# Kernel optimization log

Measured on AMD Instinct MI355X. Metric: run time of the kernel, lower is better.

The kernel has to match this reference:

```python
import jax, jax.numpy as jnp
import numpy as np

N_NODES = 50000
N_EDGES = 800000
EMB = 384            # EMBEDDING_DIM
NODE_F = EMB + 4     # 388
EDGE_F = EMB + 1     # 385
HEADS = 2
HID = 32             # per-head out_channels
HC = HEADS * HID     # 64
EDGE_IN = 2 * HC + EMB  # 512 classifier input
NEG_SLOPE = 0.2


def setup_inputs() -> dict:
    key = jax.random.key(0)
    ks = jax.random.split(key, 16)
    s = 0.05
    return {
        "x": jax.random.normal(ks[0], (N_NODES, NODE_F), dtype=jnp.float32),
        "edge_index": jax.random.randint(ks[1], (2, N_EDGES), 0, N_NODES, dtype=jnp.int32),
        "edge_attr": jax.random.uniform(ks[2], (N_EDGES, EDGE_F), dtype=jnp.float32),
        # GATv2Conv params
        "lin_l_w": jax.random.normal(ks[3], (NODE_F, HC), dtype=jnp.float32) * s,
        "lin_l_b": jnp.zeros((HC,), jnp.float32),
        "lin_r_w": jax.random.normal(ks[4], (NODE_F, HC), dtype=jnp.float32) * s,
        "lin_r_b": jnp.zeros((HC,), jnp.float32),
        "lin_e_w": jax.random.normal(ks[5], (EDGE_F, HC), dtype=jnp.float32) * s,
        "att": jax.random.normal(ks[6], (HEADS, HID), dtype=jnp.float32) * s,
        "conv_b": jnp.zeros((HC,), jnp.float32),
        # edge classifier MLP
        "mlp1_w": jax.random.normal(ks[7], (EDGE_IN, 64), dtype=jnp.float32) * s,
        "mlp1_b": jnp.zeros((64,), jnp.float32),
        "mlp2_w": jax.random.normal(ks[8], (64, 3), dtype=jnp.float32) * s,
        "mlp2_b": jnp.zeros((3,), jnp.float32),
    }


def _gatv2(x, edge_index, edge_attr, lin_l_w, lin_l_b, lin_r_w, lin_r_b,
           lin_e_w, att, conv_b):
    N = x.shape[0]
    src, tgt = edge_index[0], edge_index[1]
    # PyG add_self_loops with fill_value='mean': self-loop edge_attr is the
    # mean of incoming edge attributes per target node (0 if none).
    ones = jnp.ones((edge_attr.shape[0],), edge_attr.dtype)
    cnt = jax.ops.segment_sum(ones, tgt, num_segments=N)
    loop_attr = jax.ops.segment_sum(edge_attr, tgt, num_segments=N)
    loop_attr = loop_attr / jnp.maximum(cnt, 1.0)[:, None]
    ar = jnp.arange(N, dtype=src.dtype)
    src = jnp.concatenate([src, ar])
    tgt = jnp.concatenate([tgt, ar])
    ea = jnp.concatenate([edge_attr, loop_attr], axis=0)  # [E+N, EDGE_F]

    xl = (x @ lin_l_w + lin_l_b).reshape(N, HEADS, HID)  # source transform
    xr = (x @ lin_r_w + lin_r_b).reshape(N, HEADS, HID)  # target transform
    ee = (ea @ lin_e_w).reshape(-1, HEADS, HID)

    # GATv2 scoring: att . leaky_relu(x_j + x_i + e_ij)
    m = jax.nn.leaky_relu(xl[src] + xr[tgt] + ee, NEG_SLOPE)  # [E', H, C]
    score = jnp.einsum('ehc,hc->eh', m, att)                  # [E', H]
    # segment softmax over incoming edges of each target node
    smax = jax.ops.segment_max(score, tgt, num_segments=N)
    ex = jnp.exp(score - smax[tgt])
    ssum = jax.ops.segment_sum(ex, tgt, num_segments=N)
    alpha = ex / (ssum[tgt] + 1e-16)                          # [E', H]
    out = jax.ops.segment_sum(alpha[:, :, None] * xl[src], tgt, num_segments=N)
    return out.reshape(N, HC) + conv_b


def reference(x, edge_index, edge_attr, lin_l_w, lin_l_b, lin_r_w, lin_r_b,
              lin_e_w, att, conv_b, mlp1_w, mlp1_b, mlp2_w, mlp2_b):
    h = jax.nn.relu(_gatv2(x, edge_index, edge_attr, lin_l_w, lin_l_b,
                           lin_r_w, lin_r_b, lin_e_w, att, conv_b))
    # prediction edges == graph edges; query emb = edge_attr[:, :-1]
    src_e = h[edge_index[0]]
    tgt_e = h[edge_index[1]]
    q = edge_attr[:, :-1]
    e = jnp.concatenate([src_e, tgt_e, q], axis=1)  # [E, 512]
    e = jax.nn.relu(e @ mlp1_w + mlp1_b)
    logits = e @ mlp2_w + mlp2_b                    # [E, 3]
    probs = jax.nn.softmax(logits, axis=1)
    trust = 0.0 * probs[:, 0] + 0.5 * probs[:, 1] + 1.0 * probs[:, 2]
    return trust
```

## Files before the change

kernel.cpp:

```cpp
#include <hip/hip_runtime.h>

#define N_NODES 50000
#define N_EDGES 800000
#define NODE_F  388
#define EDGE_F  385
#define HC      64
#define KRED    384
#define NKT     6
#define NB      196

#define O_XLB     0L
#define O_XRB     1600000L
#define O_HAB     3200000L
#define O_HBB     4800000L
#define O_EESUM   6400000L
#define O_SSUM    9600000L
#define O_WSUM    9700000L
#define O_DEG     12900000L
#define O_CURSOR  12950000L
#define O_ROWPTR  13010000L
#define O_BSUM    13070000L
#define O_CSRE    13080000L
#define O_CSRS    13880000L
#define O_CSRT    14680000L
#define O_WT      15500000L
#define O_WT2     15530000L
#define O_QW      15560000L

typedef __attribute__((ext_vector_type(8))) short bf8;
typedef __attribute__((ext_vector_type(4))) float f4;

typedef __attribute__((address_space(1))) const unsigned char ga_u8;
typedef __attribute__((address_space(3))) unsigned char lds_u8;

static __device__ __forceinline__ void gload_lds16(const void* g, void* l) {
    __builtin_amdgcn_global_load_lds((ga_u8*)g, (lds_u8*)l, 16, 0, 0);
}

static __device__ __forceinline__ unsigned short f2bf(float f) {
    unsigned u = __float_as_uint(f);
    u += 0x7FFFu + ((u >> 16) & 1u);
    return (unsigned short)(u >> 16);
}
static __device__ __forceinline__ float bf2f(unsigned short h) {
    return __uint_as_float(((unsigned)h) << 16);
}
static __device__ __forceinline__ unsigned cvtpk(float lo, float hi) {
    unsigned r;
    asm("v_cvt_pk_bf16_f32 %0, %1, %2" : "=v"(r) : "v"(lo), "v"(hi));
    return r;
}
static __device__ __forceinline__ void raw_barrier() {
    __builtin_amdgcn_sched_barrier(0);
    __builtin_amdgcn_s_barrier();
    __builtin_amdgcn_sched_barrier(0);
}

__global__ __launch_bounds__(256) void k_prep(
    const float* __restrict__ we, const float* __restrict__ w1,
    const float* __restrict__ wl, const float* __restrict__ wr,
    unsigned short* __restrict__ wt, unsigned short* __restrict__ wt2)
{
    int half = blockIdx.x / 96;
    int gid = (blockIdx.x - half * 96) * 256 + threadIdx.x;
    int c  = gid / 192;
    int k  = 2 * (gid - c * 192);
    float f0, f1;
    if (half == 0) {
        if (c < HC) {
            f0 = we[(long)k * HC + c];
            f1 = we[(long)(k + 1) * HC + c];
        } else {
            f0 = w1[(long)(128 + k) * HC + (c - HC)];
            f1 = w1[(long)(128 + k + 1) * HC + (c - HC)];
        }
        *(unsigned*)(wt + (long)c * KRED + k) =
            (unsigned)f2bf(f0) | ((unsigned)f2bf(f1) << 16);
    } else {
        const float* w = (c < HC) ? wl : wr;
        int cc = (c < HC) ? c : c - HC;
        f0 = w[(long)k * HC + cc];
        f1 = w[(long)(k + 1) * HC + cc];
        *(unsigned*)(wt2 + (long)c * KRED + k) =
            (unsigned)f2bf(f0) | ((unsigned)f2bf(f1) << 16);
    }
}

__global__ __launch_bounds__(256, 5) void k_node_lin(
    const float* __restrict__ x, const unsigned short* __restrict__ wt2,
    const float* __restrict__ wl, const float* __restrict__ wr,
    const float* __restrict__ bl, const float* __restrict__ br,
    unsigned short* __restrict__ xlb, unsigned short* __restrict__ xrb)
{
    __shared__ __align__(16) char W_s[2][16384];
    const int t = threadIdx.x;
    const int l = t & 63;
    const int w = t >> 6;
    const int n0 = blockIdx.x * 64;
    const int rb = (w & 1) * 32;
    const int cb = (w >> 1) * 64;
    const int lr = l & 15;
    const int lk = l >> 4;

    int wsrc[4];
#pragma unroll
    for (int i = 0; i < 4; ++i) {
        int c = w * 32 + i * 8 + (l >> 3);
        wsrc[i] = c * (KRED * 2) + ((((l & 7) * 16)) ^ ((l >> 3) << 4));
    }
    const char* wtb = (const char*)wt2;

    long rowx[2];
#pragma unroll
    for (int rg = 0; rg < 2; ++rg) {
        int n = n0 + rb + rg * 16 + lr;
        if (n >= N_NODES) n = N_NODES - 1;
        rowx[rg] = (long)n * NODE_F;
    }

    float af[2][16];
    bf8 fa[2][2];
    f4 acc[2][4];
#pragma unroll
    for (int rg = 0; rg < 2; ++rg)
#pragma unroll
        for (int cg = 0; cg < 4; ++cg) acc[rg][cg] = (f4)(0.f);

#define STAGE_W(kt, buf)                                                         \
    {                                                                            \
        _Pragma("unroll")                                                        \
        for (int i = 0; i < 4; ++i)                                              \
            gload_lds16(wtb + wsrc[i] + (kt) * 128, &W_s[buf][w * 4096 + i * 1024]); \
    }
#define ISSUE_AX(kt)                                                             \
    {                                                                            \
        _Pragma("unroll")                                                        \
        for (int rg = 0; rg < 2; ++rg) {                                         \
            const float* rp = x + rowx[rg] + (kt) * 64 + lk * 8;                 \
            float4 a0 = *(const float4*)(rp);                                    \
            float4 a1 = *(const float4*)(rp + 4);                                \
            float4 a2 = *(const float4*)(rp + 32);                               \
            float4 a3 = *(const float4*)(rp + 36);                               \
            af[rg][0]=a0.x; af[rg][1]=a0.y; af[rg][2]=a0.z; af[rg][3]=a0.w;      \
            af[rg][4]=a1.x; af[rg][5]=a1.y; af[rg][6]=a1.z; af[rg][7]=a1.w;      \
            af[rg][8]=a2.x; af[rg][9]=a2.y; af[rg][10]=a2.z; af[rg][11]=a2.w;    \
            af[rg][12]=a3.x; af[rg][13]=a3.y; af[rg][14]=a3.z; af[rg][15]=a3.w;  \
        }                                                                        \
    }
#define CVT_AX()                                                                 \
    {                                                                            \
        _Pragma("unroll")                                                        \
        for (int rg = 0; rg < 2; ++rg)                                           \
            _Pragma("unroll")                                                    \
            for (int ks = 0; ks < 2; ++ks) {                                     \
                union { bf8 v; unsigned u[4]; } tu;                              \
                _Pragma("unroll")                                                \
                for (int p = 0; p < 4; ++p)                                      \
                    tu.u[p] = cvtpk(af[rg][ks * 8 + 2 * p], af[rg][ks * 8 + 2 * p + 1]); \
                fa[rg][ks] = tu.v;                                               \
            }                                                                    \
    }

    STAGE_W(0, 0);
    ISSUE_AX(0);

    for (int kt = 0; kt < NKT; ++kt) {
        const int buf = kt & 1;
        CVT_AX();
        if (kt < NKT - 1) { STAGE_W(kt + 1, buf ^ 1); ISSUE_AX(kt + 1); }
        raw_barrier();
        __builtin_amdgcn_s_setprio(1);
#pragma unroll
        for (int ks = 0; ks < 2; ++ks) {
            const int kb = ks * 64 + lk * 16;
#pragma unroll
            for (int cg = 0; cg < 4; ++cg) {
                const int c = cb + cg * 16 + lr;
                bf8 b = *(bf8*)(&W_s[buf][c * 128 + (kb ^ ((c & 7) << 4))]);
                acc[0][cg] = __builtin_amdgcn_mfma_f32_16x16x32_bf16(fa[0][ks], b, acc[0][cg], 0, 0, 0);
                acc[1][cg] = __builtin_amdgcn_mfma_f32_16x16x32_bf16(fa[1][ks], b, acc[1][cg], 0, 0, 0);
            }
        }
        __builtin_amdgcn_s_setprio(0);
        raw_barrier();
    }

    const float* wsf = (cb == 0) ? wl : wr;
    const float* bsf = (cb == 0) ? bl : br;
    unsigned short* dst = (cb == 0) ? xlb : xrb;
    float wtail[4][4], bias[4];
#pragma unroll
    for (int cg = 0; cg < 4; ++cg) {
        int c = cg * 16 + lr;
        bias[cg] = bsf[c];
#pragma unroll
        for (int j = 0; j < 4; ++j)
            wtail[j][cg] = wsf[(long)(KRED + j) * HC + c];
    }
#pragma unroll
    for (int rg = 0; rg < 2; ++rg)
#pragma unroll
    for (int r = 0; r < 4; ++r) {
        const int n = n0 + rb + rg * 16 + lk * 4 + r;
        const int nc = (n < N_NODES) ? n : N_NODES - 1;
        float4 xt = *(const float4*)(x + (long)nc * NODE_F + KRED);
#pragma unroll
        for (int cg = 0; cg < 4; ++cg) {
            float v = acc[rg][cg][r] + bias[cg]
                    + xt.x * wtail[0][cg] + xt.y * wtail[1][cg]
                    + xt.z * wtail[2][cg] + xt.w * wtail[3][cg];
            float nb = __shfl_xor(v, 1);
            if (!(lr & 1) && n < N_NODES)
                *(unsigned*)&dst[(long)n * HC + cg * 16 + lr] = cvtpk(v, nb);
        }
    }
#undef STAGE_W
#undef ISSUE_AX
#undef CVT_AX
}

__global__ __launch_bounds__(256) void k_hist(const int* __restrict__ ei, int* __restrict__ deg)
{
    int e = blockIdx.x * 256 + threadIdx.x;
    if (e < N_EDGES) atomicAdd(&deg[ei[N_EDGES + e]], 1);
}

__global__ __launch_bounds__(256) void k_scan_bsum(const int* __restrict__ deg, int* __restrict__ bsum)
{
    __shared__ int red[4];
    int i = blockIdx.x * 256 + threadIdx.x;
    int v = (i < N_NODES) ? deg[i] : 0;
    for (int m = 1; m < 64; m <<= 1) v += __shfl_xor(v, m);
    if ((threadIdx.x & 63) == 0) red[threadIdx.x >> 6] = v;
    __syncthreads();
    if (threadIdx.x == 0) bsum[blockIdx.x] = red[0] + red[1] + red[2] + red[3];
}

__global__ __launch_bounds__(256) void k_scan_boff(int* bsum)
{
    __shared__ int sc[256];
    int t = threadIdx.x;
    int v = (t < NB) ? bsum[t] : 0;
    sc[t] = v; __syncthreads();
    for (int off = 1; off < 256; off <<= 1) {
        int tv = (t >= off) ? sc[t - off] : 0;
        __syncthreads();
        sc[t] += tv;
        __syncthreads();
    }
    if (t < NB) bsum[t] = sc[t] - v;
}

__global__ __launch_bounds__(256) void k_scan_row(const int* __restrict__ deg,
                                                  const int* __restrict__ bsum,
                                                  int* __restrict__ rowptr)
{
    __shared__ int sc[256];
    int t = threadIdx.x;
    int i = blockIdx.x * 256 + t;
    int v = (i < N_NODES) ? deg[i] : 0;
    sc[t] = v; __syncthreads();
    for (int off = 1; off < 256; off <<= 1) {
        int tv = (t >= off) ? sc[t - off] : 0;
        __syncthreads();
        sc[t] += tv;
        __syncthreads();
    }
    if (i < N_NODES) rowptr[i] = bsum[blockIdx.x] + sc[t] - v;
    if (i == N_NODES - 1) rowptr[N_NODES] = N_EDGES;
}

__global__ __launch_bounds__(256) void k_scatter(const int* __restrict__ ei,
                                                 const int* __restrict__ rowptr,
                                                 int* __restrict__ cursor,
                                                 int* __restrict__ csr_e, int* __restrict__ csr_s,
                                                 int* __restrict__ csr_t)
{
    int e = blockIdx.x * 256 + threadIdx.x;
    if (e >= N_EDGES) return;
    int g = ei[N_EDGES + e];
    int pos = rowptr[g] + atomicAdd(&cursor[g], 1);
    csr_e[pos] = e;
    csr_s[pos] = ei[e];
    csr_t[pos] = g;
}

__global__ __launch_bounds__(256, 4) void k_edge_main(
    const float* __restrict__ ea,
    const int* __restrict__ csr_e, const int* __restrict__ csr_s, const int* __restrict__ csr_t,
    const unsigned short* __restrict__ wt, const float* __restrict__ we,
    const unsigned short* __restrict__ xlb, const unsigned short* __restrict__ xrb,
    const float* __restrict__ att,
    float* __restrict__ eesum, float* __restrict__ ssum, float* __restrict__ wsum,
    unsigned short* __restrict__ qWP)
{
    __shared__ __align__(16) char lds[32768];
    const int t = threadIdx.x;
    const int l = t & 63;
    const int w = t >> 6;
    const long pb = (long)blockIdx.x * 64;
    const int rb = (w & 1) * 32;
    const int cb = (w >> 1) * 64;
    const int lr = l & 15;
    const int lk = l >> 4;

    int wsrc[4];
#pragma unroll
    for (int i = 0; i < 4; ++i) {
        int c = w * 32 + i * 8 + (l >> 3);
        wsrc[i] = c * (KRED * 2) + ((((l & 7) * 16)) ^ ((l >> 3) << 4));
    }
    const char* wtb = (const char*)wt;

    unsigned rowb[2];
#pragma unroll
    for (int rg = 0; rg < 2; ++rg) {
        int e = csr_e[pb + rb + rg * 16 + lr];
        rowb[rg] = (unsigned)e * EDGE_F;
    }

    float af[2][2][16];
    bf8 fa[2][2];
    f4 acc[2][4];
#pragma unroll
    for (int rg = 0; rg < 2; ++rg)
#pragma unroll
        for (int cg = 0; cg < 4; ++cg) acc[rg][cg] = (f4)(0.f);

#define STAGE_W(kt, buf)                                                         \
    {                                                                            \
        _Pragma("unroll")                                                        \
        for (int i = 0; i < 4; ++i)                                              \
            gload_lds16(wtb + wsrc[i] + (kt) * 128,                              \
                        &lds[(buf) * 16384 + w * 4096 + i * 1024]);              \
    }

#define ISSUE_A(b, kt)                                                           \
    {                                                                            \
        _Pragma("unroll")                                                        \
        for (int rg = 0; rg < 2; ++rg) {                                         \
            const float* rp = ea + rowb[rg] + (kt) * 64 + lk * 8;                \
            _Pragma("unroll")                                                    \
            for (int q4 = 0; q4 < 4; ++q4)                                       \
                __builtin_memcpy(&af[b][rg][q4 * 4],                             \
                                 rp + (q4 >> 1) * 32 + (q4 & 1) * 4, 16);        \
        }                                                                        \
    }

#define CVT_A(b)                                                                 \
    {                                                                            \
        _Pragma("unroll")                                                        \
        for (int rg = 0; rg < 2; ++rg)                                           \
            _Pragma("unroll")                                                    \
            for (int ks = 0; ks < 2; ++ks) {                                     \
                union { bf8 v; unsigned u[4]; } tu;                              \
                _Pragma("unroll")                                                \
                for (int p = 0; p < 4; ++p)                                      \
                    tu.u[p] = cvtpk(af[b][rg][ks * 8 + 2 * p],                   \
                                    af[b][rg][ks * 8 + 2 * p + 1]);              \
                fa[rg][ks] = tu.v;                                               \
            }                                                                    \
    }

    STAGE_W(0, 0); ISSUE_A(0, 0);
    STAGE_W(1, 1); ISSUE_A(1, 1);

    for (int kt = 0; kt < NKT; ++kt) {
        const int sl = kt & 1;
        CVT_A(sl);
        raw_barrier();
        __builtin_amdgcn_s_setprio(1);
#pragma unroll
        for (int ks = 0; ks < 2; ++ks) {
            const int kb = ks * 64 + lk * 16;
#pragma unroll
            for (int cg = 0; cg < 4; ++cg) {
                const int c = cb + cg * 16 + lr;
                bf8 b = *(bf8*)(&lds[sl * 16384 + c * 128 + (kb ^ ((c & 7) << 4))]);
                acc[0][cg] = __builtin_amdgcn_mfma_f32_16x16x32_bf16(fa[0][ks], b, acc[0][cg], 0, 0, 0);
                acc[1][cg] = __builtin_amdgcn_mfma_f32_16x16x32_bf16(fa[1][ks], b, acc[1][cg], 0, 0, 0);
            }
        }
        __builtin_amdgcn_s_setprio(0);
        raw_barrier();
        if (kt + 2 < NKT) {
            STAGE_W(kt + 2, sl);
            ISSUE_A(sl, kt + 2);
        }
    }

    float (*ee_s)[65] = (float(*)[65])lds;
    int*   tgt_s      = (int*)(lds + 16640);
    float (*ex_s)[2]  = (float(*)[2])(lds + 16896);

    if (cb == 0) {
        float attv[4], w384[4];
#pragma unroll
        for (int cg = 0; cg < 4; ++cg) {
            attv[cg] = att[cg * 16 + lr];
            w384[cg] = we[(long)(EDGE_F - 1) * HC + cg * 16 + lr];
        }
#pragma unroll
        for (int rg = 0; rg < 2; ++rg)
#pragma unroll
        for (int r = 0; r < 4; ++r) {
            const int row = rb + rg * 16 + lk * 4 + r;
            const long p = pb + row;
            const int s = csr_s[p];
            const int g = csr_t[p];
            const float a384 = ea[(long)csr_e[p] * EDGE_F + (EDGE_F - 1)];
            float sc0 = 0.f, sc1 = 0.f;
#pragma unroll
            for (int cg = 0; cg < 4; ++cg) {
                const int c = cg * 16 + lr;
                float eev = fmaf(a384, w384[cg], acc[rg][cg][r]);
                ee_s[row][c] = eev;
                float m = eev + bf2f(xlb[(long)s * HC + c]) + bf2f(xrb[(long)g * HC + c]);
                float lv = m > 0.f ? m : 0.2f * m;
                float tm = lv * attv[cg];
                if (cg < 2) sc0 += tm; else sc1 += tm;
            }
            sc0 += __shfl_xor(sc0, 1); sc0 += __shfl_xor(sc0, 2);
            sc0 += __shfl_xor(sc0, 4); sc0 += __shfl_xor(sc0, 8);
            sc1 += __shfl_xor(sc1, 1); sc1 += __shfl_xor(sc1, 2);
            sc1 += __shfl_xor(sc1, 4); sc1 += __shfl_xor(sc1, 8);
            if (lr == 0) {
                ex_s[row][0] = __expf(sc0);
                tgt_s[row] = g;
            } else if (lr == 1) {
                ex_s[row][1] = __expf(sc1);
            }
        }
    } else {
#pragma unroll
        for (int rg = 0; rg < 2; ++rg)
#pragma unroll
        for (int r = 0; r < 4; ++r) {
            const long p = pb + rb + rg * 16 + lk * 4 + r;
#pragma unroll
            for (int cg = 0; cg < 4; ++cg) {
                float v = acc[rg][cg][r];
                float nb = __shfl_xor(v, 1);
                if (!(lr & 1)) {
                    unsigned pk = cvtpk(v, nb);
                    *(unsigned*)&qWP[p * HC + cg * 16 + lr] = pk;
                }
            }
        }
    }
    __syncthreads();

    {
        const int c = t & 63;
        const int q = t >> 6;
        const int r0 = q * 16;
        int   cur = tgt_s[r0];
        float run = ee_s[r0][c];
        for (int r = r0 + 1; r < r0 + 16; ++r) {
            int tg = tgt_s[r];
            if (tg != cur) {
                atomicAdd(&eesum[(long)cur * HC + c], run);
                run = 0.f; cur = tg;
            }
            run += ee_s[r][c];
        }
        atomicAdd(&eesum[(long)cur * HC + c], run);
        if (c < 2) {
            int   cur2 = tgt_s[r0];
            float run2 = ex_s[r0][c];
            for (int r = r0 + 1; r < r0 + 16; ++r) {
                int tg = tgt_s[r];
                if (tg != cur2) {
                    atomicAdd(&ssum[(long)cur2 * 2 + c], run2);
                    run2 = 0.f; cur2 = tg;
                }
                run2 += ex_s[r][c];
            }
            atomicAdd(&ssum[(long)cur2 * 2 + c], run2);
        }
    }
    __syncthreads();

    if (cb == 0) {
#pragma unroll
        for (int rg = 0; rg < 2; ++rg)
#pragma unroll
        for (int r = 0; r < 4; ++r) {
            const int row = rb + rg * 16 + lk * 4 + r;
            const long p = pb + row;
            const int s = csr_s[p];
            const float ex0 = ex_s[row][0];
            const float ex1 = ex_s[row][1];
#pragma unroll
            for (int cg = 0; cg < 4; ++cg) {
                const int c = cg * 16 + lr;
                float xv = bf2f(xlb[(long)s * HC + c]);
                ee_s[row][c] = (cg < 2 ? ex0 : ex1) * xv;
            }
        }
    }
    __syncthreads();

    {
        const int c = t & 63;
        const int q = t >> 6;
        const int r0 = q * 16;
        int   cur = tgt_s[r0];
        float run = ee_s[r0][c];
        for (int r = r0 + 1; r < r0 + 16; ++r) {
            int tg = tgt_s[r];
            if (tg != cur) {
                atomicAdd(&wsum[(long)cur * HC + c], run);
                run = 0.f; cur = tg;
            }
            run += ee_s[r][c];
        }
        atomicAdd(&wsum[(long)cur * HC + c], run);
    }
#undef STAGE_W
#undef ISSUE_A
#undef CVT_A
}

__global__ __launch_bounds__(256) void k_node_agg(
    const int* __restrict__ rowptr,
    const float* __restrict__ eesum, const float* __restrict__ ssum,
    const float* __restrict__ wsum,
    const unsigned short* __restrict__ xlb, const unsigned short* __restrict__ xrb,
    const float* __restrict__ att, const float* __restrict__ convb,
    const float* __restrict__ w1,
    unsigned short* __restrict__ hAb, unsigned short* __restrict__ hBb)
{
    const int lane = threadIdx.x & 63;
    const int n = blockIdx.x * 4 + (threadIdx.x >> 6);
    if (n >= N_NODES) return;
    const int h = lane >> 5;
    const int deg = rowptr[n + 1] - rowptr[n];

    float eeS = eesum[(long)n * HC + lane] / (deg > 0 ? (float)deg : 1.f);
    float sex = ssum[(long)n * 2 + h];

    float xlv = bf2f(xlb[(long)n * HC + lane]);
    float v = xlv + bf2f(xrb[(long)n * HC + lane]) + eeS;
    float lv = v > 0.f ? v : 0.2f * v;
    float partial = lv * att[lane];
    partial += __shfl_xor(partial, 1);
    partial += __shfl_xor(partial, 2);
    partial += __shfl_xor(partial, 4);
    partial += __shfl_xor(partial, 8);
    partial += __shfl_xor(partial, 16);
    float exSelf = __expf(partial);
    float inv = 1.f / (sex + exSelf + 1e-16f);
    float aggr = (exSelf * xlv + wsum[(long)n * HC + lane]) * inv;

    float hv = fmaxf(aggr + convb[lane], 0.f);
    float accA = 0.f, accB = 0.f;
    for (int k = 0; k < 64; ++k) {
        float hb = __shfl(hv, k);
        accA = fmaf(hb, w1[k * HC + lane], accA);
        accB = fmaf(hb, w1[(64 + k) * HC + lane], accB);
    }
    hAb[(long)n * HC + lane] = f2bf(accA);
    hBb[(long)n * HC + lane] = f2bf(accB);
}

__global__ __launch_bounds__(256) void k_trust(
    const int* __restrict__ csr_e, const int* __restrict__ csr_s, const int* __restrict__ csr_t,
    const unsigned short* __restrict__ hAb, const unsigned short* __restrict__ hBb,
    const unsigned short* __restrict__ qWP, const float* __restrict__ b1,
    const float* __restrict__ w2, const float* __restrict__ b2,
    float* __restrict__ out)
{
    const long p = (long)blockIdx.x * 256 + threadIdx.x;
    const int s = csr_s[p];
    const int g = csr_t[p];
    const uint4* ha = (const uint4*)(hAb + (long)s * HC);
    const uint4* hb = (const uint4*)(hBb + (long)g * HC);
    const uint4* qw = (const uint4*)(qWP + p * HC);
    float a0 = 0.f, a1 = 0.f, a2 = 0.f;
#pragma unroll
    for (int ch = 0; ch < 8; ++ch) {
        uint4 ua = ha[ch], ub = hb[ch], uq = qw[ch];
        const unsigned* pa = (const unsigned*)&ua;
        const unsigned* pbb = (const unsigned*)&ub;
        const unsigned* pq = (const unsigned*)&uq;
#pragma unroll
        for (int j = 0; j < 4; ++j) {
            const int c = ch * 8 + j * 2;
            unsigned va = pa[j], vb = pbb[j], vq = pq[j];
            float m0 = __uint_as_float(va << 16) + __uint_as_float(vb << 16)
                     + __uint_as_float(vq << 16) + b1[c];
            float m1 = __uint_as_float(va & 0xffff0000u) + __uint_as_float(vb & 0xffff0000u)
                     + __uint_as_float(vq & 0xffff0000u) + b1[c + 1];
            m0 = fmaxf(m0, 0.f);
            m1 = fmaxf(m1, 0.f);
            a0 = fmaf(m0, w2[c * 3 + 0], a0); a0 = fmaf(m1, w2[c * 3 + 3], a0);
            a1 = fmaf(m0, w2[c * 3 + 1], a1); a1 = fmaf(m1, w2[c * 3 + 4], a1);
            a2 = fmaf(m0, w2[c * 3 + 2], a2); a2 = fmaf(m1, w2[c * 3 + 5], a2);
        }
    }
    float l0 = a0 + b2[0], l1 = a1 + b2[1], l2 = a2 + b2[2];
    float mx = fmaxf(l0, fmaxf(l1, l2));
    float e0 = __expf(l0 - mx), e1 = __expf(l1 - mx), e2 = __expf(l2 - mx);
    out[csr_e[p]] = (0.5f * e1 + e2) / (e0 + e1 + e2);
}

extern "C" void kernel_launch(void* const* d_in, const int* in_sizes, int n_in,
                              void* d_out, int out_size, void* d_ws, size_t ws_size,
                              hipStream_t stream)
{
    (void)in_sizes; (void)n_in; (void)out_size; (void)ws_size;
    const float* x     = (const float*)d_in[0];
    const int*   ei    = (const int*)  d_in[1];
    const float* ea    = (const float*)d_in[2];
    const float* wl    = (const float*)d_in[3];
    const float* bl    = (const float*)d_in[4];
    const float* wr    = (const float*)d_in[5];
    const float* br    = (const float*)d_in[6];
    const float* we    = (const float*)d_in[7];
    const float* att   = (const float*)d_in[8];
    const float* convb = (const float*)d_in[9];
    const float* w1    = (const float*)d_in[10];
    const float* b1    = (const float*)d_in[11];
    const float* w2    = (const float*)d_in[12];
    const float* b2    = (const float*)d_in[13];

    float* ws = (float*)d_ws;
    unsigned short* xlb = (unsigned short*)(ws + O_XLB);
    unsigned short* xrb = (unsigned short*)(ws + O_XRB);
    unsigned short* hAb = (unsigned short*)(ws + O_HAB);
    unsigned short* hBb = (unsigned short*)(ws + O_HBB);
    float* eesum  = ws + O_EESUM;
    float* ssum   = ws + O_SSUM;
    float* wsum   = ws + O_WSUM;
    unsigned short* wt  = (unsigned short*)(ws + O_WT);
    unsigned short* wt2 = (unsigned short*)(ws + O_WT2);
    int* deg    = (int*)(ws + O_DEG);
    int* cursor = (int*)(ws + O_CURSOR);
    int* rowptr = (int*)(ws + O_ROWPTR);
    int* bsum   = (int*)(ws + O_BSUM);
    int* csr_e  = (int*)(ws + O_CSRE);
    int* csr_s  = (int*)(ws + O_CSRS);
    int* csr_t  = (int*)(ws + O_CSRT);
    unsigned short* qWP = (unsigned short*)(ws + O_QW);
    float* out  = (float*)d_out;

    hipMemsetAsync(ws + O_EESUM, 0, (size_t)(13000000L - O_EESUM) * sizeof(float), stream);

    k_prep<<<192, 256, 0, stream>>>(we, w1, wl, wr, wt, wt2);
    k_hist<<<3125, 256, 0, stream>>>(ei, deg);
    k_scan_bsum<<<NB, 256, 0, stream>>>(deg, bsum);
    k_scan_boff<<<1, 256, 0, stream>>>(bsum);
    k_scan_row<<<NB, 256, 0, stream>>>(deg, bsum, rowptr);
    k_scatter<<<3125, 256, 0, stream>>>(ei, rowptr, cursor, csr_e, csr_s, csr_t);
    k_node_lin<<<782, 256, 0, stream>>>(x, wt2, wl, wr, bl, br, xlb, xrb);
    k_edge_main<<<N_EDGES / 64, 256, 0, stream>>>(ea, csr_e, csr_s, csr_t, wt, we,
                                                  xlb, xrb, att, eesum, ssum, wsum, qWP);
    k_node_agg<<<N_NODES / 4, 256, 0, stream>>>(rowptr, eesum, ssum, wsum,
                                                xlb, xrb, att, convb, w1, hAb, hBb);
    k_trust<<<3125, 256, 0, stream>>>(csr_e, csr_s, csr_t, hAb, hBb, qWP,
                                      b1, w2, b2, out);
}
```

Before: 749.5 us.

## Merge prep/hist and scan kernels, pack CSR arrays into int4 records

```diff
diff --git a/kernel.cpp b/kernel.cpp
--- a/kernel.cpp
+++ b/kernel.cpp
@@ -20,12 +20,10 @@
 #define O_CURSOR  12950000L
 #define O_ROWPTR  13010000L
 #define O_BSUM    13070000L
-#define O_CSRE    13080000L
-#define O_CSRS    13880000L
-#define O_CSRT    14680000L
-#define O_WT      15500000L
-#define O_WT2     15530000L
-#define O_QW      15560000L
+#define O_CSREST  13080000L
+#define O_WT      16300000L
+#define O_WT2     16330000L
+#define O_QW      16360000L
 
 typedef __attribute__((ext_vector_type(8))) short bf8;
 typedef __attribute__((ext_vector_type(4))) float f4;
@@ -56,11 +54,18 @@
     __builtin_amdgcn_sched_barrier(0);
 }
 
-__global__ __launch_bounds__(256) void k_prep(
+__global__ __launch_bounds__(256) void k_prep_hist(
     const float* __restrict__ we, const float* __restrict__ w1,
     const float* __restrict__ wl, const float* __restrict__ wr,
-    unsigned short* __restrict__ wt, unsigned short* __restrict__ wt2)
-{
+    const int* __restrict__ ei,
+    unsigned short* __restrict__ wt, unsigned short* __restrict__ wt2,
+    int* __restrict__ deg)
+{
+    if (blockIdx.x >= 192) {
+        int e = (blockIdx.x - 192) * 256 + threadIdx.x;
+        if (e < N_EDGES) atomicAdd(&deg[ei[N_EDGES + e]], 1);
+        return;
+    }
     int half = blockIdx.x / 96;
     int gid = (blockIdx.x - half * 96) * 256 + threadIdx.x;
     int c  = gid / 192;
@@ -219,12 +224,6 @@
 #undef CVT_AX
 }
 
-__global__ __launch_bounds__(256) void k_hist(const int* __restrict__ ei, int* __restrict__ deg)
-{
-    int e = blockIdx.x * 256 + threadIdx.x;
-    if (e < N_EDGES) atomicAdd(&deg[ei[N_EDGES + e]], 1);
-}
-
 __global__ __launch_bounds__(256) void k_scan_bsum(const int* __restrict__ deg, int* __restrict__ bsum)
 {
     __shared__ int red[4];
@@ -236,58 +235,45 @@
     if (threadIdx.x == 0) bsum[blockIdx.x] = red[0] + red[1] + red[2] + red[3];
 }
 
-__global__ __launch_bounds__(256) void k_scan_boff(int* bsum)
+__global__ __launch_bounds__(256) void k_scan_row(const int* __restrict__ deg,
+                                                  const int* __restrict__ bsum,
+                                                  int* __restrict__ rowptr)
 {
     __shared__ int sc[256];
+    __shared__ int red[4];
     int t = threadIdx.x;
-    int v = (t < NB) ? bsum[t] : 0;
+    int bv = (t < NB && t < (int)blockIdx.x) ? bsum[t] : 0;
+    for (int m = 1; m < 64; m <<= 1) bv += __shfl_xor(bv, m);
+    if ((t & 63) == 0) red[t >> 6] = bv;
+    int i = blockIdx.x * 256 + t;
+    int v = (i < N_NODES) ? deg[i] : 0;
     sc[t] = v; __syncthreads();
+    int base = red[0] + red[1] + red[2] + red[3];
     for (int off = 1; off < 256; off <<= 1) {
         int tv = (t >= off) ? sc[t - off] : 0;
         __syncthreads();
         sc[t] += tv;
         __syncthreads();
     }
-    if (t < NB) bsum[t] = sc[t] - v;
-}
-
-__global__ __launch_bounds__(256) void k_scan_row(const int* __restrict__ deg,
-                                                  const int* __restrict__ bsum,
-                                                  int* __restrict__ rowptr)
-{
-    __shared__ int sc[256];
-    int t = threadIdx.x;
-    int i = blockIdx.x * 256 + t;
-    int v = (i < N_NODES) ? deg[i] : 0;
-    sc[t] = v; __syncthreads();
-    for (int off = 1; off < 256; off <<= 1) {
-        int tv = (t >= off) ? sc[t - off] : 0;
-        __syncthreads();
-        sc[t] += tv;
-        __syncthreads();
-    }
-    if (i < N_NODES) rowptr[i] = bsum[blockIdx.x] + sc[t] - v;
+    if (i < N_NODES) rowptr[i] = base + sc[t] - v;
     if (i == N_NODES - 1) rowptr[N_NODES] = N_EDGES;
 }
 
 __global__ __launch_bounds__(256) void k_scatter(const int* __restrict__ ei,
                                                  const int* __restrict__ rowptr,
                                                  int* __restrict__ cursor,
-                                                 int* __restrict__ csr_e, int* __restrict__ csr_s,
-                                                 int* __restrict__ csr_t)
+                                                 int4* __restrict__ csr_est)
 {
     int e = blockIdx.x * 256 + threadIdx.x;
     if (e >= N_EDGES) return;
     int g = ei[N_EDGES + e];
     int pos = rowptr[g] + atomicAdd(&cursor[g], 1);
-    csr_e[pos] = e;
-    csr_s[pos] = ei[e];
-    csr_t[pos] = g;
+    int4 v; v.x = e; v.y = ei[e]; v.z = g; v.w = 0;
+    csr_est[pos] = v;
 }
 
 __global__ __launch_bounds__(256, 4) void k_edge_main(
-    const float* __restrict__ ea,
-    const int* __restrict__ csr_e, const int* __restrict__ csr_s, const int* __restrict__ csr_t,
+    const float* __restrict__ ea, const int4* __restrict__ csr_est,
     const unsigned short* __restrict__ wt, const float* __restrict__ we,
     const unsigned short* __restrict__ xlb, const unsigned short* __restrict__ xrb,
     const float* __restrict__ att,
@@ -315,7 +301,7 @@
     unsigned rowb[2];
 #pragma unroll
     for (int rg = 0; rg < 2; ++rg) {
-        int e = csr_e[pb + rb + rg * 16 + lr];
+        int e = csr_est[pb + rb + rg * 16 + lr].x;
         rowb[rg] = (unsigned)e * EDGE_F;
     }
 
@@ -406,9 +392,10 @@
         for (int r = 0; r < 4; ++r) {
             const int row = rb + rg * 16 + lk * 4 + r;
             const long p = pb + row;
-            const int s = csr_s[p];
-            const int g = csr_t[p];
-            const float a384 = ea[(long)csr_e[p] * EDGE_F + (EDGE_F - 1)];
+            const int4 est = csr_est[p];
+            const int s = est.y;
+            const int g = est.z;
+            const float a384 = ea[(long)est.x * EDGE_F + (EDGE_F - 1)];
             float sc0 = 0.f, sc1 = 0.f;
 #pragma unroll
             for (int cg = 0; cg < 4; ++cg) {
@@ -488,7 +475,7 @@
         for (int r = 0; r < 4; ++r) {
             const int row = rb + rg * 16 + lk * 4 + r;
             const long p = pb + row;
-            const int s = csr_s[p];
+            const int s = csr_est[p].y;
             const float ex0 = ex_s[row][0];
             const float ex1 = ex_s[row][1];
 #pragma unroll
@@ -565,15 +552,16 @@
 }
 
 __global__ __launch_bounds__(256) void k_trust(
-    const int* __restrict__ csr_e, const int* __restrict__ csr_s, const int* __restrict__ csr_t,
+    const int4* __restrict__ csr_est,
     const unsigned short* __restrict__ hAb, const unsigned short* __restrict__ hBb,
     const unsigned short* __restrict__ qWP, const float* __restrict__ b1,
     const float* __restrict__ w2, const float* __restrict__ b2,
     float* __restrict__ out)
 {
     const long p = (long)blockIdx.x * 256 + threadIdx.x;
-    const int s = csr_s[p];
-    const int g = csr_t[p];
+    const int4 est = csr_est[p];
+    const int s = est.y;
+    const int g = est.z;
     const uint4* ha = (const uint4*)(hAb + (long)s * HC);
     const uint4* hb = (const uint4*)(hBb + (long)g * HC);
     const uint4* qw = (const uint4*)(qWP + p * HC);
@@ -602,7 +590,7 @@
     float l0 = a0 + b2[0], l1 = a1 + b2[1], l2 = a2 + b2[2];
     float mx = fmaxf(l0, fmaxf(l1, l2));
     float e0 = __expf(l0 - mx), e1 = __expf(l1 - mx), e2 = __expf(l2 - mx);
-    out[csr_e[p]] = (0.5f * e1 + e2) / (e0 + e1 + e2);
+    out[est.x] = (0.5f * e1 + e2) / (e0 + e1 + e2);
 }
 
 extern "C" void kernel_launch(void* const* d_in, const int* in_sizes, int n_in,
@@ -639,25 +627,20 @@
     int* cursor = (int*)(ws + O_CURSOR);
     int* rowptr = (int*)(ws + O_ROWPTR);
     int* bsum   = (int*)(ws + O_BSUM);
-    int* csr_e  = (int*)(ws + O_CSRE);
-    int* csr_s  = (int*)(ws + O_CSRS);
-    int* csr_t  = (int*)(ws + O_CSRT);
+    int4* csr_est = (int4*)(ws + O_CSREST);
     unsigned short* qWP = (unsigned short*)(ws + O_QW);
     float* out  = (float*)d_out;
 
     hipMemsetAsync(ws + O_EESUM, 0, (size_t)(13000000L - O_EESUM) * sizeof(float), stream);
 
-    k_prep<<<192, 256, 0, stream>>>(we, w1, wl, wr, wt, wt2);
-    k_hist<<<3125, 256, 0, stream>>>(ei, deg);
+    k_prep_hist<<<3317, 256, 0, stream>>>(we, w1, wl, wr, ei, wt, wt2, deg);
     k_scan_bsum<<<NB, 256, 0, stream>>>(deg, bsum);
-    k_scan_boff<<<1, 256, 0, stream>>>(bsum);
     k_scan_row<<<NB, 256, 0, stream>>>(deg, bsum, rowptr);
-    k_scatter<<<3125, 256, 0, stream>>>(ei, rowptr, cursor, csr_e, csr_s, csr_t);
+    k_scatter<<<3125, 256, 0, stream>>>(ei, rowptr, cursor, csr_est);
     k_node_lin<<<782, 256, 0, stream>>>(x, wt2, wl, wr, bl, br, xlb, xrb);
-    k_edge_main<<<N_EDGES / 64, 256, 0, stream>>>(ea, csr_e, csr_s, csr_t, wt, we,
+    k_edge_main<<<N_EDGES / 64, 256, 0, stream>>>(ea, csr_est, wt, we,
                                                   xlb, xrb, att, eesum, ssum, wsum, qWP);
     k_node_agg<<<N_NODES / 4, 256, 0, stream>>>(rowptr, eesum, ssum, wsum,
                                                 xlb, xrb, att, convb, w1, hAb, hBb);
-    k_trust<<<3125, 256, 0, stream>>>(csr_e, csr_s, csr_t, hAb, hBb, qWP,
-                                      b1, w2, b2, out);
-}
+    k_trust<<<3125, 256, 0, stream>>>(csr_est, hAb, hBb, qWP, b1, w2, b2, out);
+}
```

After: 725.5 us. 1.03x faster.
